# Kernel optimization log

Hardware: AMD Instinct MI355X
Metric: run time of the kernel (lower is better)

## Reference

```python
import jax, jax.numpy as jnp
import numpy as np

B, T, N, C = 16, 12, 2048, 64
WIN = 3                    # window_size
F = 3                      # len(filters) branches
NW = T - WIN + 1           # number of windows = 10


def setup_inputs() -> dict:
    key = jax.random.key(0)
    k0, k1, k2, k3, k4 = jax.random.split(key, 5)
    data = jax.random.normal(k0, (B, T, N, C), jnp.float32)
    # scale adj so aggregated features stay O(1)
    adj = jax.random.normal(k1, (WIN * N, WIN * N), jnp.float32) / np.float32(np.sqrt(WIN * N))
    temporal_emb = jax.random.normal(k2, (1, T, 1, C), jnp.float32) * 0.1
    spatial_emb = jax.random.normal(k3, (1, 1, N, C), jnp.float32) * 0.1
    # per-window, per-filter GLU linear: C -> 2C
    W = jax.random.normal(k4, (NW, F, C, 2 * C), jnp.float32) / np.float32(np.sqrt(C))
    b = jnp.zeros((NW, F, 2 * C), jnp.float32)
    return {"data": data, "adj": adj, "temporal_emb": temporal_emb,
            "spatial_emb": spatial_emb, "W": W, "b": b}


def reference(data, adj, temporal_emb, spatial_emb, W, b):
    # data: (B,T,N,C); adj: (3N,3N)
    x = data + temporal_emb + spatial_emb                     # (B,T,N,C)
    # sliding windows of 3 time steps, flattened to 3N nodes  # (B,NW,3N,C)
    wins = jnp.stack([x[:, i:i + WIN].reshape(B, WIN * N, C) for i in range(NW)], axis=1)
    # only the middle N rows of the bmm output survive the mid-step slice,
    # so aggregate with just those rows of adj (same math, less work)
    adj_mid = adj[(WIN - 1) // 2 * N:(WIN + 1) // 2 * N]      # (N, 3N)
    agg = jnp.einsum('mn,bwnc->bwmc', adj_mid, wins)          # (B,NW,N,C)
    # per-window per-filter linear C -> 2C, then GLU
    pre = jnp.einsum('bwnc,wfcd->bwfnd', agg, W) + b[None, :, :, None, :]  # (B,NW,F,N,2C)
    lhs, rhs = jnp.split(pre, 2, axis=-1)
    glu = lhs * jax.nn.sigmoid(rhs)                           # (B,NW,F,N,C)
    # max over filter branches -> (B, T-2, N, C)
    return jnp.max(glu, axis=2)
```

## Files before the change

kernel.cpp:

```cpp
#include <hip/hip_runtime.h>
#include <hip/hip_bf16.h>

#define B_ 16
#define T_ 12
#define N_ 2048
#define C_ 64
#define NW_ 10
#define K_ 6144

#define NT2_ 96
#define ABUF_E 16384
#define BUF2_E 36864

typedef __attribute__((ext_vector_type(8))) short bf16x8;
typedef __attribute__((ext_vector_type(4))) float f32x4;

__device__ __forceinline__ unsigned short f2bf(float f) {
  union { float f; unsigned int u; } v; v.f = f;
  unsigned int u = v.u;
  return (unsigned short)((u + 0x7FFFu + ((u >> 16) & 1u)) >> 16);
}

__device__ __forceinline__ void gload16(const void* g, void* l) {
  __builtin_amdgcn_global_load_lds(
      (const __attribute__((address_space(1))) unsigned int*)g,
      (__attribute__((address_space(3))) unsigned int*)l, 16, 0, 0);
}

template<int N>
__device__ __forceinline__ void vmw() {
  if constexpr (N == 5)      asm volatile("s_waitcnt vmcnt(5)" ::: "memory");
  else if constexpr (N == 4) asm volatile("s_waitcnt vmcnt(4)" ::: "memory");
  else                       asm volatile("s_waitcnt vmcnt(0)" ::: "memory");
}

__global__ __launch_bounds__(256) void prep_x2(const float* __restrict__ data,
                                               const float* __restrict__ temb,
                                               const float* __restrict__ semb,
                                               unsigned short* __restrict__ xbt2) {
  int idx = blockIdx.x * 256 + threadIdx.x;
  int q = idx & 511;
  int btnb = idx >> 9;
  int nb = btnb & 31;
  int bt = btnb >> 5;
  int t = bt % T_;
  int o = q >> 6, c = q & 63;
  int n0 = nb * 64 + o * 8;
  float te = temb[t * C_ + c];
  union { unsigned short s[8]; uint4 v; } pk;
#pragma unroll
  for (int e = 0; e < 8; ++e) {
    int n = n0 + e;
    float d = data[((size_t)bt * N_ + n) * C_ + c];
    float se = semb[(size_t)n * C_ + c];
    pk.s[e] = f2bf(d + te + se);
  }
  *(uint4*)(xbt2 + (size_t)idx * 8) = pk.v;
}

__global__ __launch_bounds__(256) void prep_adj2(const float* __restrict__ adj,
                                                 unsigned short* __restrict__ adjb2) {
  int idx = blockIdx.x * 256 + threadIdx.x;
  int s = idx & 2047;
  int bmt = idx >> 11;
  int t = bmt % NT2_;
  int bm = bmt / NT2_;
  int r = s & 15;
  int o = (s >> 4) & 7;
  int rg = s >> 7;
  int m = bm * 256 + rg * 16 + r;
  int k = t * 64 + o * 8;
  const float* src = adj + ((size_t)(N_ + m)) * K_ + k;
  float4 a = *(const float4*)src;
  float4 b4 = *(const float4*)(src + 4);
  union { unsigned short s8[8]; uint4 v; } pk;
  pk.s8[0] = f2bf(a.x);  pk.s8[1] = f2bf(a.y);  pk.s8[2] = f2bf(a.z);  pk.s8[3] = f2bf(a.w);
  pk.s8[4] = f2bf(b4.x); pk.s8[5] = f2bf(b4.y); pk.s8[6] = f2bf(b4.z); pk.s8[7] = f2bf(b4.w);
  *(uint4*)(adjb2 + (size_t)idx * 8) = pk.v;
}

__global__ __launch_bounds__(256) void prep_w(const float* __restrict__ W,
                                              unsigned short* __restrict__ wbt) {
  int idx = blockIdx.x * 256 + threadIdx.x;
  int c = idx & 63;
  int d = (idx >> 6) & 127;
  int wf = idx >> 13;
  float v = W[((size_t)wf * 64 + c) * 128 + d];
  wbt[idx] = f2bf(v);
}

struct SegCtx {
  const unsigned short* Abase;
  const unsigned short* Xroot;
  int lane, wid, wm, wn, l4, l15, fbase, bOffLane;
};

__device__ __forceinline__ void stage_group(const SegCtx& s, unsigned short* lds, int t, int kh) {
  unsigned short* buf = lds + (t & 1) * BUF2_E;
  int tp = t >> 5, nn = t & 31;
#pragma unroll
  for (int ci = 0; ci < 2; ++ci) {
    int rg = s.wid * 2 + ci;
    int off = (rg * 128 + kh * 64) * 8;
    gload16(s.Abase + (size_t)t * ABUF_E + off + s.lane * 8, buf + off);
  }
  unsigned short* Bb = buf + ABUF_E;
  const unsigned short* Xr = s.Xroot + ((size_t)tp * 32 + nn) * 4096;
  int c0 = (s.wid < 4) ? s.wid * 3 : 12 + (s.wid - 4) * 2;
  int nc = (s.wid < 4) ? 3 : 2;
  for (int ci = 0; ci < nc; ++ci) {
    int cg = c0 + ci;
    gload16(Xr + (size_t)(cg >> 2) * 131072 + kh * 2048 + (cg & 3) * 128 + s.bOffLane,
            Bb + cg * 1024 + kh * 512);
  }
}

__device__ __forceinline__ void vm_steady(const SegCtx& s) {
  if (s.wid < 4) vmw<5>(); else vmw<4>();
}

template<int KK>
__device__ __forceinline__ void phase_body(const SegCtx& s, unsigned short* lds, int t,
                                           bf16x8 (&curLo)[4], bf16x8 (&nxtLo)[4],
                                           f32x4 (&acc)[8][5]) {
  if (t == NT2_ - 1) vmw<0>(); else vm_steady(s);
  __builtin_amdgcn_s_barrier();
  __builtin_amdgcn_sched_barrier(0);
  if constexpr (KK == 0) { if (t + 1 < NT2_) stage_group(s, lds, t + 1, 1); }
  else                   { if (t + 2 < NT2_) stage_group(s, lds, t + 2, 0); }
  unsigned short* buf = lds + (t & 1) * BUF2_E;
  const unsigned short* Ab = buf;
  const unsigned short* Bb = buf + ABUF_E;
  bf16x8 bfv[5], afhi[4];
#pragma unroll
  for (int c = 0; c < 5; ++c)
    bfv[c] = *(const bf16x8*)(Bb + (s.wn * 5 + c) * 1024 + KK * 512 + s.fbase);
#pragma unroll
  for (int i = 0; i < 4; ++i)
    afhi[i] = *(const bf16x8*)(Ab + (s.wm * 8 + 4 + i) * 1024 + KK * 512 + s.fbase);
  if constexpr (KK == 0) {
#pragma unroll
    for (int i = 0; i < 4; ++i)
      nxtLo[i] = *(const bf16x8*)(Ab + (s.wm * 8 + i) * 1024 + 512 + s.fbase);
  } else {
    if (t + 1 < NT2_) {
      const unsigned short* nb = lds + ((t + 1) & 1) * BUF2_E;
#pragma unroll
      for (int i = 0; i < 4; ++i)
        nxtLo[i] = *(const bf16x8*)(nb + (s.wm * 8 + i) * 1024 + s.fbase);
    }
  }
  __builtin_amdgcn_s_setprio(1);
#pragma unroll
  for (int i = 0; i < 4; ++i)
#pragma unroll
    for (int c = 0; c < 5; ++c)
      acc[i][c] = __builtin_amdgcn_mfma_f32_16x16x32_bf16(curLo[i], bfv[c], acc[i][c], 0, 0, 0);
#pragma unroll
  for (int i = 0; i < 4; ++i)
#pragma unroll
    for (int c = 0; c < 5; ++c)
      acc[4 + i][c] = __builtin_amdgcn_mfma_f32_16x16x32_bf16(afhi[i], bfv[c], acc[4 + i][c], 0, 0, 0);
  __builtin_amdgcn_s_setprio(0);
  __builtin_amdgcn_sched_barrier(0);
}

__global__ __launch_bounds__(512, 2) void gemm_agg(const unsigned short* __restrict__ adjb2,
                                                   const unsigned short* __restrict__ xbt2,
                                                   unsigned short* __restrict__ aggb) {
  __shared__ __align__(16) unsigned short lds[2 * BUF2_E];
  int bid = blockIdx.x;
  int bm = bid & 7;
  int rest = bid >> 3;
  int seg = rest & 1;
  int b = rest >> 1;
  int w0 = seg * 5;
  int tid = threadIdx.x;
  SegCtx s;
  s.lane = tid & 63; s.wid = tid >> 6;
  s.wm = s.wid >> 2; s.wn = s.wid & 3;
  s.l4 = s.lane >> 4; s.l15 = s.lane & 15;
  s.fbase = s.l4 * 128 + s.l15 * 8;
  s.bOffLane = s.l4 * 512 + s.l15 * 8;
  s.Abase = adjb2 + (size_t)bm * NT2_ * ABUF_E;
  s.Xroot = xbt2 + ((size_t)(b * T_ + w0)) * 32 * 4096;

  f32x4 acc[8][5];
#pragma unroll
  for (int i = 0; i < 8; ++i)
#pragma unroll
    for (int c = 0; c < 5; ++c) acc[i][c] = (f32x4)0.f;

  __builtin_amdgcn_sched_barrier(0);
  stage_group(s, lds, 0, 0);
  stage_group(s, lds, 0, 1);
  stage_group(s, lds, 1, 0);
  vm_steady(s);
  __builtin_amdgcn_s_barrier();
  __builtin_amdgcn_sched_barrier(0);

  bf16x8 P[4], Q[4];
#pragma unroll
  for (int i = 0; i < 4; ++i)
    P[i] = *(const bf16x8*)(lds + (s.wm * 8 + i) * 1024 + s.fbase);

  for (int t = 0; t < NT2_; ++t) {
    phase_body<0>(s, lds, t, P, Q, acc);
    phase_body<1>(s, lds, t, Q, P, acc);
  }

  unsigned short* Ob0 = aggb + (size_t)(b * NW_ + w0) * N_ * C_;
#pragma unroll
  for (int c = 0; c < 5; ++c) {
    int col = s.wn * 80 + c * 16 + s.l15;
    int g = col >> 6, cc = col & 63;
    unsigned short* Ob = Ob0 + (size_t)g * N_ * C_ + cc;
#pragma unroll
    for (int i = 0; i < 8; ++i) {
      int n0 = bm * 256 + s.wm * 128 + i * 16 + s.l4 * 4;
#pragma unroll
      for (int q = 0; q < 4; ++q)
        Ob[(size_t)(n0 + q) * C_] = f2bf(acc[i][c][q]);
    }
  }
}

__global__ __launch_bounds__(256) void glu_out(const unsigned short* __restrict__ aggb,
                                               const unsigned short* __restrict__ wbt,
                                               const float* __restrict__ bias,
                                               float* __restrict__ out) {
  __shared__ __align__(16) unsigned short sW[3 * 128 * 64];
  int bn = blockIdx.x, bw = blockIdx.y;
  int w = bw % NW_;
  int tid = threadIdx.x, lane = tid & 63, wid = tid >> 6;
  int lrow8 = lane >> 3, jl = lane & 7;
  int l15 = lane & 15, l4 = lane >> 4;
  const unsigned short* Wsrc = wbt + (size_t)w * 3 * 128 * 64;
  for (int ci = 0; ci < 12; ++ci) {
    int chunk = wid * 12 + ci;
    int row = chunk * 8 + lrow8;
    int jg = jl ^ (row & 7);
    gload16(Wsrc + (size_t)row * 64 + jg * 8, &sW[chunk * 512]);
  }
  const unsigned short* Abase = aggb + ((size_t)bw * N_ + bn * 128 + wid * 32) * C_;
  bf16x8 af[2][2];
  for (int i = 0; i < 2; ++i)
    for (int kh = 0; kh < 2; ++kh)
      af[i][kh] = *(const bf16x8*)(Abase + (size_t)(i * 16 + l15) * C_ + kh * 32 + l4 * 8);
  __syncthreads();

  float omax[2][4][4];
  for (int i = 0; i < 2; ++i)
    for (int j = 0; j < 4; ++j)
      for (int r = 0; r < 4; ++r) omax[i][j][r] = -INFINITY;

  for (int f = 0; f < 3; ++f) {
    f32x4 acc[2][8];
    for (int i = 0; i < 2; ++i)
      for (int j = 0; j < 8; ++j) acc[i][j] = (f32x4)0.f;
    for (int kh = 0; kh < 2; ++kh) {
      int gchunk = kh * 4 + l4;
      for (int j = 0; j < 8; ++j) {
        int row = f * 128 + j * 16 + l15;
        int ch = gchunk ^ (row & 7);
        bf16x8 bfr = *(const bf16x8*)&sW[row * 64 + ch * 8];
        for (int i = 0; i < 2; ++i)
          acc[i][j] = __builtin_amdgcn_mfma_f32_16x16x32_bf16(af[i][kh], bfr, acc[i][j], 0, 0, 0);
      }
    }
    for (int j = 0; j < 4; ++j) {
      float bl = bias[(w * 3 + f) * 128 + j * 16 + l15];
      float br = bias[(w * 3 + f) * 128 + 64 + j * 16 + l15];
      for (int i = 0; i < 2; ++i)
        for (int r = 0; r < 4; ++r) {
          float lhs = acc[i][j][r] + bl;
          float rhs = acc[i][j + 4][r] + br;
          float g = lhs / (1.f + __expf(-rhs));
          omax[i][j][r] = fmaxf(omax[i][j][r], g);
        }
    }
  }
  float* Obase = out + ((size_t)bw * N_ + bn * 128 + wid * 32) * C_;
  for (int i = 0; i < 2; ++i)
    for (int j = 0; j < 4; ++j)
      for (int r = 0; r < 4; ++r)
        Obase[(size_t)(i * 16 + l4 * 4 + r) * C_ + j * 16 + l15] = omax[i][j][r];
}

extern "C" void kernel_launch(void* const* d_in, const int* in_sizes, int n_in,
                              void* d_out, int out_size, void* d_ws, size_t ws_size,
                              hipStream_t stream) {
  const float* data = (const float*)d_in[0];
  const float* adj  = (const float*)d_in[1];
  const float* temb = (const float*)d_in[2];
  const float* semb = (const float*)d_in[3];
  const float* W    = (const float*)d_in[4];
  const float* bias = (const float*)d_in[5];
  float* out = (float*)d_out;

  char* ws = (char*)d_ws;
  unsigned short* xbt2  = (unsigned short*)ws;
  unsigned short* adjb2 = (unsigned short*)(ws + 50331648);
  unsigned short* wbt   = (unsigned short*)(ws + 75497472);
  unsigned short* aggb  = (unsigned short*)(ws + 75988992);

  hipLaunchKernelGGL(prep_x2,   dim3(12288), dim3(256), 0, stream, data, temb, semb, xbt2);
  hipLaunchKernelGGL(prep_adj2, dim3(6144),  dim3(256), 0, stream, adj, adjb2);
  hipLaunchKernelGGL(prep_w,    dim3(960),   dim3(256), 0, stream, W, wbt);
  hipLaunchKernelGGL(gemm_agg,  dim3(256),   dim3(512), 0, stream, adjb2, xbt2, aggb);
  hipLaunchKernelGGL(glu_out,   dim3(16, 160), dim3(256), 0, stream, aggb, wbt, bias, out);
}
```

Measured before the change: 325.1 us.

## Load B operand directly into registers, stage only adj tiles in LDS

After: 331.7 us. 2.0% more time.

```diff
diff --git a/kernel.cpp b/kernel.cpp
--- a/kernel.cpp
+++ b/kernel.cpp
@@ -10,7 +10,8 @@
 
 #define NT2_ 96
 #define ABUF_E 16384
-#define BUF2_E 36864
+#define NT32 192
+#define ALDS 8192
 
 typedef __attribute__((ext_vector_type(8))) short bf16x8;
 typedef __attribute__((ext_vector_type(4))) float f32x4;
@@ -29,9 +30,8 @@
 
 template<int N>
 __device__ __forceinline__ void vmw() {
-  if constexpr (N == 5)      asm volatile("s_waitcnt vmcnt(5)" ::: "memory");
-  else if constexpr (N == 4) asm volatile("s_waitcnt vmcnt(4)" ::: "memory");
-  else                       asm volatile("s_waitcnt vmcnt(0)" ::: "memory");
+  if constexpr (N == 5) asm volatile("s_waitcnt vmcnt(5)" ::: "memory");
+  else                  asm volatile("s_waitcnt vmcnt(0)" ::: "memory");
 }
 
 __global__ __launch_bounds__(256) void prep_x2(const float* __restrict__ data,
@@ -91,84 +91,64 @@
 
 struct SegCtx {
   const unsigned short* Abase;
-  const unsigned short* Xroot;
-  int lane, wid, wm, wn, l4, l15, fbase, bOffLane;
+  const unsigned short* Xlane;
+  int lane, wid, wm, wn, l4, l15, fbase;
+  int bcoff[5];
 };
 
-__device__ __forceinline__ void stage_group(const SegCtx& s, unsigned short* lds, int t, int kh) {
-  unsigned short* buf = lds + (t & 1) * BUF2_E;
-  int tp = t >> 5, nn = t & 31;
+__device__ __forceinline__ void stage_A(const SegCtx& s, unsigned short* ldsA, int u) {
+  const unsigned short* src = s.Abase + (size_t)(u >> 1) * ABUF_E + (u & 1) * 512;
+  unsigned short* dst = ldsA + (u & 1) * ALDS;
 #pragma unroll
   for (int ci = 0; ci < 2; ++ci) {
     int rg = s.wid * 2 + ci;
-    int off = (rg * 128 + kh * 64) * 8;
-    gload16(s.Abase + (size_t)t * ABUF_E + off + s.lane * 8, buf + off);
-  }
-  unsigned short* Bb = buf + ABUF_E;
-  const unsigned short* Xr = s.Xroot + ((size_t)tp * 32 + nn) * 4096;
-  int c0 = (s.wid < 4) ? s.wid * 3 : 12 + (s.wid - 4) * 2;
-  int nc = (s.wid < 4) ? 3 : 2;
-  for (int ci = 0; ci < nc; ++ci) {
-    int cg = c0 + ci;
-    gload16(Xr + (size_t)(cg >> 2) * 131072 + kh * 2048 + (cg & 3) * 128 + s.bOffLane,
-            Bb + cg * 1024 + kh * 512);
-  }
-}
-
-__device__ __forceinline__ void vm_steady(const SegCtx& s) {
-  if (s.wid < 4) vmw<5>(); else vmw<4>();
-}
-
-template<int KK>
-__device__ __forceinline__ void phase_body(const SegCtx& s, unsigned short* lds, int t,
-                                           bf16x8 (&curLo)[4], bf16x8 (&nxtLo)[4],
-                                           f32x4 (&acc)[8][5]) {
-  if (t == NT2_ - 1) vmw<0>(); else vm_steady(s);
-  __builtin_amdgcn_s_barrier();
-  __builtin_amdgcn_sched_barrier(0);
-  if constexpr (KK == 0) { if (t + 1 < NT2_) stage_group(s, lds, t + 1, 1); }
-  else                   { if (t + 2 < NT2_) stage_group(s, lds, t + 2, 0); }
-  unsigned short* buf = lds + (t & 1) * BUF2_E;
-  const unsigned short* Ab = buf;
-  const unsigned short* Bb = buf + ABUF_E;
-  bf16x8 bfv[5], afhi[4];
-#pragma unroll
-  for (int c = 0; c < 5; ++c)
-    bfv[c] = *(const bf16x8*)(Bb + (s.wn * 5 + c) * 1024 + KK * 512 + s.fbase);
+    gload16(src + rg * 1024 + s.lane * 8, dst + rg * 512);
+  }
+}
+
+__device__ __forceinline__ void phase32(const SegCtx& s, unsigned short* ldsA, int u,
+                                        bf16x8 (&Bc)[5], bf16x8 (&Bn)[5],
+                                        f32x4 (&acc)[8][5]) {
+  if (u + 1 < NT32) {
+    stage_A(s, ldsA, u + 1);
+    const unsigned short* Bu = s.Xlane + (size_t)(u + 1) * 2048;
+#pragma unroll
+    for (int c = 0; c < 5; ++c)
+      Bn[c] = *(const bf16x8*)(Bu + s.bcoff[c]);
+  }
+  const unsigned short* Ab = ldsA + (u & 1) * ALDS + s.wm * 4096 + s.fbase;
+  bf16x8 af[4];
+#pragma unroll
+  for (int i = 0; i < 4; ++i) af[i] = *(const bf16x8*)(Ab + i * 512);
+  __builtin_amdgcn_s_setprio(1);
 #pragma unroll
   for (int i = 0; i < 4; ++i)
-    afhi[i] = *(const bf16x8*)(Ab + (s.wm * 8 + 4 + i) * 1024 + KK * 512 + s.fbase);
-  if constexpr (KK == 0) {
-#pragma unroll
-    for (int i = 0; i < 4; ++i)
-      nxtLo[i] = *(const bf16x8*)(Ab + (s.wm * 8 + i) * 1024 + 512 + s.fbase);
-  } else {
-    if (t + 1 < NT2_) {
-      const unsigned short* nb = lds + ((t + 1) & 1) * BUF2_E;
-#pragma unroll
-      for (int i = 0; i < 4; ++i)
-        nxtLo[i] = *(const bf16x8*)(nb + (s.wm * 8 + i) * 1024 + s.fbase);
-    }
-  }
+#pragma unroll
+    for (int c = 0; c < 5; ++c)
+      acc[i][c] = __builtin_amdgcn_mfma_f32_16x16x32_bf16(af[i], Bc[c], acc[i][c], 0, 0, 0);
+  __builtin_amdgcn_s_setprio(0);
+  bf16x8 ah[4];
+#pragma unroll
+  for (int i = 0; i < 4; ++i) ah[i] = *(const bf16x8*)(Ab + (4 + i) * 512);
   __builtin_amdgcn_s_setprio(1);
 #pragma unroll
   for (int i = 0; i < 4; ++i)
 #pragma unroll
     for (int c = 0; c < 5; ++c)
-      acc[i][c] = __builtin_amdgcn_mfma_f32_16x16x32_bf16(curLo[i], bfv[c], acc[i][c], 0, 0, 0);
-#pragma unroll
-  for (int i = 0; i < 4; ++i)
-#pragma unroll
-    for (int c = 0; c < 5; ++c)
-      acc[4 + i][c] = __builtin_amdgcn_mfma_f32_16x16x32_bf16(afhi[i], bfv[c], acc[4 + i][c], 0, 0, 0);
+      acc[4 + i][c] = __builtin_amdgcn_mfma_f32_16x16x32_bf16(ah[i], Bc[c], acc[4 + i][c], 0, 0, 0);
   __builtin_amdgcn_s_setprio(0);
-  __builtin_amdgcn_sched_barrier(0);
+  if (u < NT32 - 1) {
+    if (u < NT32 - 2) vmw<5>();
+    else vmw<0>();
+    __builtin_amdgcn_s_barrier();
+    __builtin_amdgcn_sched_barrier(0);
+  }
 }
 
 __global__ __launch_bounds__(512, 2) void gemm_agg(const unsigned short* __restrict__ adjb2,
                                                    const unsigned short* __restrict__ xbt2,
                                                    unsigned short* __restrict__ aggb) {
-  __shared__ __align__(16) unsigned short lds[2 * BUF2_E];
+  __shared__ __align__(16) unsigned short ldsA[2 * ALDS];
   int bid = blockIdx.x;
   int bm = bid & 7;
   int rest = bid >> 3;
@@ -181,9 +161,13 @@
   s.wm = s.wid >> 2; s.wn = s.wid & 3;
   s.l4 = s.lane >> 4; s.l15 = s.lane & 15;
   s.fbase = s.l4 * 128 + s.l15 * 8;
-  s.bOffLane = s.l4 * 512 + s.l15 * 8;
   s.Abase = adjb2 + (size_t)bm * NT2_ * ABUF_E;
-  s.Xroot = xbt2 + ((size_t)(b * T_ + w0)) * 32 * 4096;
+  s.Xlane = xbt2 + ((size_t)(b * T_ + w0)) * C_ * N_ + s.l4 * 512 + s.l15 * 8;
+#pragma unroll
+  for (int c = 0; c < 5; ++c) {
+    int cg = s.wn * 5 + c;
+    s.bcoff[c] = (cg >> 2) * 131072 + (cg & 3) * 128;
+  }
 
   f32x4 acc[8][5];
 #pragma unroll
@@ -191,22 +175,19 @@
 #pragma unroll
     for (int c = 0; c < 5; ++c) acc[i][c] = (f32x4)0.f;
 
+  bf16x8 Br0[5], Br1[5];
   __builtin_amdgcn_sched_barrier(0);
-  stage_group(s, lds, 0, 0);
-  stage_group(s, lds, 0, 1);
-  stage_group(s, lds, 1, 0);
-  vm_steady(s);
+#pragma unroll
+  for (int c = 0; c < 5; ++c)
+    Br0[c] = *(const bf16x8*)(s.Xlane + s.bcoff[c]);
+  stage_A(s, ldsA, 0);
+  vmw<0>();
   __builtin_amdgcn_s_barrier();
   __builtin_amdgcn_sched_barrier(0);
 
-  bf16x8 P[4], Q[4];
-#pragma unroll
-  for (int i = 0; i < 4; ++i)
-    P[i] = *(const bf16x8*)(lds + (s.wm * 8 + i) * 1024 + s.fbase);
-
-  for (int t = 0; t < NT2_; ++t) {
-    phase_body<0>(s, lds, t, P, Q, acc);
-    phase_body<1>(s, lds, t, Q, P, acc);
+  for (int u = 0; u < NT32; u += 2) {
+    phase32(s, ldsA, u, Br0, Br1, acc);
+    phase32(s, ldsA, u + 1, Br1, Br0, acc);
   }
 
   unsigned short* Ob0 = aggb + (size_t)(b * NW_ + w0) * N_ * C_;
```
